# Performance work log

Measured on AMD Instinct MI355X. Metric: run time of the kernel, lower is better.

## Reference

```python
import jax, jax.numpy as jnp
import numpy as np

B, S, E, H = 2, 2048, 1024, 16
D = E // H


def setup_inputs() -> dict:
    key = jax.random.key(0)
    ks = jax.random.split(key, 12)
    init = lambda k, shp: (jax.random.normal(k, shp, dtype=jnp.float32) * 0.02)
    return {
        "q": jax.random.normal(ks[0], (B, S, E), dtype=jnp.float32),
        "k": jax.random.normal(ks[1], (B, S, E), dtype=jnp.float32),
        "v": jax.random.normal(ks[2], (B, S, E), dtype=jnp.float32),
        "wq": init(ks[3], (E, E)), "bq": jnp.zeros((E,), jnp.float32),
        "wk": init(ks[4], (E, E)), "bk": jnp.zeros((E,), jnp.float32),
        "wv": init(ks[5], (E, E)), "bv": jnp.zeros((E,), jnp.float32),
        "wo": init(ks[6], (E, E)), "bo": jnp.zeros((E,), jnp.float32),
        "gamma": jnp.ones((E,), jnp.float32),
        "beta": jnp.zeros((E,), jnp.float32),
        "mask": 1,
    }


def _split_heads(x):
    # [B,S,E] -> [B,H,S,D]
    return x.reshape(x.shape[0], x.shape[1], H, D).transpose(0, 2, 1, 3)


def _mha(q, k, v, wq, bq, wk, bk, wv, bv, wo, bo, gamma, beta, causal):
    residual = q
    query = _split_heads(q @ wq + bq)
    key = _split_heads(k @ wk + bk)
    value = _split_heads(v @ wv + bv)
    scale = jnp.sqrt(jnp.float32(D)) + 1e-8  # matches torch: sqrt(dk) + 1e-8
    score = jnp.einsum("bhqd,bhkd->bhqk", query, key) / scale
    if causal:
        cm = jnp.tril(jnp.ones((S, S), dtype=bool))  # 1 - triu(...,1)
        score = jnp.where(cm[None, None], score, -jnp.inf)
    attn = jax.nn.softmax(score, axis=-1)
    ctx = jnp.einsum("bhqk,bhkd->bhqd", attn, value)
    ctx = ctx.transpose(0, 2, 1, 3).reshape(ctx.shape[0], S, E)
    o = ctx @ wo + bo  # dropout is identity in eval mode
    x = residual + o
    mu = jnp.mean(x, axis=-1, keepdims=True)
    var = jnp.var(x, axis=-1, keepdims=True)
    return (x - mu) / jnp.sqrt(var + 1e-5) * gamma + beta


def reference(q, k, v, wq, bq, wk, bk, wv, bv, wo, bo, gamma, beta, mask):
    return _mha(q, k, v, wq, bq, wk, bk, wv, bv, wo, bo, gamma, beta, bool(mask))
```

## Files before the change

kernel.cpp:

```cpp
#include <hip/hip_runtime.h>
#include <hip/hip_bf16.h>

typedef __bf16 bf16x8 __attribute__((ext_vector_type(8)));
typedef __attribute__((ext_vector_type(8))) short short8_t;
typedef __attribute__((ext_vector_type(4))) short short4_t;
typedef __attribute__((ext_vector_type(4))) float f32x4;

#define DEV __device__ __forceinline__

constexpr int Bc = 2, Sc = 2048, Ec = 1024, Hc = 16, Dc = 64;
constexpr int Mc = Bc * Sc;
constexpr int NT = Sc / 64;
constexpr float kQS = (float)((1.0 / (8.0 + 1e-8)) * 1.4426950408889634);

DEV short f2bf(float f) {
  unsigned int u = __builtin_bit_cast(unsigned int, f);
  unsigned int r = u + 0x7fffu + ((u >> 16) & 1u);
  return (short)(r >> 16);
}
DEV short bfc(float f) { __bf16 h = (__bf16)f; return __builtin_bit_cast(short, h); }

DEV float fexp2(float x) {
#if __has_builtin(__builtin_amdgcn_exp2f)
  return __builtin_amdgcn_exp2f(x);
#else
  float r;
  asm("v_exp_f32 %0, %1" : "=v"(r) : "v"(x));
  return r;
#endif
}

DEV void gload16(const short* g, short* lds) {
  __builtin_amdgcn_global_load_lds((const __attribute__((address_space(1))) void*)g,
                                   (__attribute__((address_space(3))) void*)lds, 16, 0, 0);
}

struct Prep {
  const float* w[4]; short* wt[4];
  const float* x[3]; short* y[3];
};
__global__ __launch_bounds__(256) void k_prep(Prep a) {
  const int bid = blockIdx.x;
  if (bid < 4096) {
    __shared__ float tile[32][33];
    const int z = bid >> 10, bk = (bid >> 5) & 31, bn = bid & 31;
    const float* w = a.w[z];
    short* wt = a.wt[z];
    int tx = threadIdx.x & 31, ty = threadIdx.x >> 5;
#pragma unroll
    for (int i = 0; i < 4; i++)
      tile[ty + i * 8][tx] = w[(size_t)(bk * 32 + ty + i * 8) * Ec + bn * 32 + tx];
    __syncthreads();
#pragma unroll
    for (int i = 0; i < 4; i++)
      wt[(size_t)(bn * 32 + ty + i * 8) * Ec + bk * 32 + tx] = f2bf(tile[tx][ty + i * 8]);
  } else {
    const int idx = bid - 4096;
    const int z = idx >> 11, c = idx & 2047;
    const float* x = a.x[z];
    short* y = a.y[z];
    size_t i = ((size_t)c * 256 + threadIdx.x) * 8;
    float4 v0 = *(const float4*)(x + i);
    float4 v1 = *(const float4*)(x + i + 4);
    short8_t h;
    h[0] = bfc(v0.x); h[1] = bfc(v0.y); h[2] = bfc(v0.z); h[3] = bfc(v0.w);
    h[4] = bfc(v1.x); h[5] = bfc(v1.y); h[6] = bfc(v1.z); h[7] = bfc(v1.w);
    *(short8_t*)(y + i) = h;
  }
}

DEV void gemm_mfma(const short* lA, const short* lB, f32x4 (&acc)[4][4], int lane, int wm, int wn) {
#pragma unroll
  for (int kc = 0; kc < 2; kc++) {
    bf16x8 a[4], b[4];
#pragma unroll
    for (int mf = 0; mf < 4; mf++) {
      int row = wm * 64 + mf * 16 + (lane & 15);
      int ch = (kc * 4 + (lane >> 4)) ^ (row & 7);
      a[mf] = *(const bf16x8*)&lA[row * 64 + (ch << 3)];
    }
#pragma unroll
    for (int nf = 0; nf < 4; nf++) {
      int row = wn * 64 + nf * 16 + (lane & 15);
      int ch = (kc * 4 + (lane >> 4)) ^ (row & 7);
      b[nf] = *(const bf16x8*)&lB[row * 64 + (ch << 3)];
    }
#pragma unroll
    for (int mf = 0; mf < 4; mf++)
#pragma unroll
      for (int nf = 0; nf < 4; nf++)
        acc[mf][nf] = __builtin_amdgcn_mfma_f32_16x16x32_bf16(a[mf], b[nf], acc[mf][nf], 0, 0, 0);
  }
}

struct QKV3 { const short* A[3]; const short* Bt[3]; const float* bias[3]; short* out[3]; };

__global__ __launch_bounds__(256) void k_gemm_qkv(QKV3 args) {
  __shared__ short lA[2][128 * 64];
  __shared__ short lB[2][128 * 64];
  int lin = blockIdx.x + 8 * blockIdx.y + 256 * blockIdx.z;
  lin = (lin & 7) * 96 + (lin >> 3);
  const int bx = lin & 7, by = (lin >> 3) & 31, z = lin >> 8;
  const short* A = args.A[z];
  const short* Bt = args.Bt[z];
  const float* bias = args.bias[z];
  short* out = args.out[z];
  const int t = threadIdx.x;
  const int m0 = by * 128, n0 = bx * 128;
  const int lane = t & 63, wid = t >> 6;
  const int wm = wid >> 1, wn = wid & 1;
  const int rl = lane >> 3, chs = ((lane & 7) ^ rl) << 3;

  f32x4 acc[4][4];
#pragma unroll
  for (int i = 0; i < 4; i++)
#pragma unroll
    for (int j = 0; j < 4; j++) acc[i][j] = {0.f, 0.f, 0.f, 0.f};

  auto stage = [&](int k0, int buf) {
#pragma unroll
    for (int j = 0; j < 4; j++) {
      int r0 = wid * 32 + j * 8;
      gload16(A + (size_t)(m0 + r0 + rl) * Ec + k0 + chs, &lA[buf][r0 * 64]);
      gload16(Bt + (size_t)(n0 + r0 + rl) * Ec + k0 + chs, &lB[buf][r0 * 64]);
    }
  };
  stage(0, 0);
  __syncthreads();
  int buf = 0;
  for (int s = 0; s < Ec / 64; s++) {
    if (s + 1 < Ec / 64) stage((s + 1) * 64, buf ^ 1);
    gemm_mfma(lA[buf], lB[buf], acc, lane, wm, wn);
    __syncthreads();
    buf ^= 1;
  }
#pragma unroll
  for (int mf = 0; mf < 4; mf++) {
#pragma unroll
    for (int nf = 0; nf < 4; nf++) {
      int col = n0 + wn * 64 + nf * 16 + (lane & 15);
      float bs = bias[col];
      int row0 = m0 + wm * 64 + mf * 16 + ((lane >> 4) << 2);
      int bh = ((row0 >> 11) << 4) + (col >> 6);
      int d = col & 63;
      size_t bhbase = (size_t)bh * Sc * Dc;
      if (z == 0) {
#pragma unroll
        for (int r = 0; r < 4; r++) {
          int row = row0 + r;
          size_t off = bhbase + (size_t)(row & 2047) * Dc + d;
          out[off] = f2bf((acc[mf][nf][r] + bs) * kQS);
        }
      } else if (z == 1) {
#pragma unroll
        for (int r = 0; r < 4; r++) {
          int s = (row0 + r) & 2047;
          size_t off = bhbase + (size_t)(s >> 4) * 1024 + ((d >> 5) * 512) +
                       (((d >> 3) & 3) * 128) + ((s & 15) * 8) + (d & 7);
          out[off] = f2bf(acc[mf][nf][r] + bs);
        }
      } else {
        short4_t h;
#pragma unroll
        for (int r = 0; r < 4; r++) h[r] = f2bf(acc[mf][nf][r] + bs);
        int s0 = row0 & 2047;
        size_t off = bhbase + (size_t)(s0 >> 6) * 4096 + (((s0 >> 5) & 1) * 2048) +
                     (((d >> 4) & 3) * 512) + ((((s0 >> 3) & 3) * 16 + (d & 15)) * 8) + (s0 & 7);
        *(short4_t*)&out[off] = h;
      }
    }
  }
}

__global__ __launch_bounds__(256) void k_gemm_o(const short* __restrict__ A,
                                                const short* __restrict__ Bt,
                                                const float* __restrict__ bias,
                                                const float* __restrict__ res,
                                                float* __restrict__ out) {
  __shared__ short lA[2][128 * 64];
  __shared__ short lB[2][128 * 64];
  int lin = blockIdx.x + 8 * blockIdx.y;
  lin = (lin & 7) * 32 + (lin >> 3);
  const int bx = lin & 7, by = lin >> 3;
  const int t = threadIdx.x;
  const int m0 = by * 128, n0 = bx * 128;
  const int lane = t & 63, wid = t >> 6;
  const int wm = wid >> 1, wn = wid & 1;
  const int rl = lane >> 3, chs = ((lane & 7) ^ rl) << 3;

  f32x4 acc[4][4];
#pragma unroll
  for (int i = 0; i < 4; i++)
#pragma unroll
    for (int j = 0; j < 4; j++) acc[i][j] = {0.f, 0.f, 0.f, 0.f};

  auto stage = [&](int k0, int buf) {
#pragma unroll
    for (int j = 0; j < 4; j++) {
      int r0 = wid * 32 + j * 8;
      gload16(A + (size_t)(m0 + r0 + rl) * Ec + k0 + chs, &lA[buf][r0 * 64]);
      gload16(Bt + (size_t)(n0 + r0 + rl) * Ec + k0 + chs, &lB[buf][r0 * 64]);
    }
  };
  stage(0, 0);
  __syncthreads();
  int buf = 0;
  for (int s = 0; s < Ec / 64; s++) {
    if (s + 1 < Ec / 64) stage((s + 1) * 64, buf ^ 1);
    gemm_mfma(lA[buf], lB[buf], acc, lane, wm, wn);
    __syncthreads();
    buf ^= 1;
  }
#pragma unroll
  for (int mf = 0; mf < 4; mf++) {
#pragma unroll
    for (int nf = 0; nf < 4; nf++) {
      int col = n0 + wn * 64 + nf * 16 + (lane & 15);
      float bs = bias[col];
#pragma unroll
      for (int r = 0; r < 4; r++) {
        int row = m0 + wm * 64 + mf * 16 + ((lane >> 4) << 2) + r;
        out[(size_t)row * Ec + col] = acc[mf][nf][r] + bs + res[(size_t)row * Ec + col];
      }
    }
  }
}

__global__ __launch_bounds__(256, 3) void k_attn7(const short* __restrict__ Qp,
                                                  const short* __restrict__ Kf,
                                                  const short* __restrict__ Vf,
                                                  const int* __restrict__ maskp,
                                                  short* __restrict__ ctx) {
  __shared__ short lP[64 * 64];
  const int lin = blockIdx.x;
  const int bh = lin & 31;
  const int qtord = lin >> 5;
  const int qt = (qtord & 8) ? (qtord ^ 7) : qtord;
  const int t = threadIdx.x, lane = t & 63, w = t >> 6;
  const int gs = lane >> 4, l15 = lane & 15;
  const bool causal = maskp[0] != 0;
  const int b = bh >> 4, h = bh & 15;
  const size_t base = (size_t)bh * Sc * Dc;
  const int ktend = causal ? qt : (NT - 1);

  bf16x8 aq[2];
  {
    const short* qptr = Qp + base + (size_t)(qt * 64 + w * 16 + l15) * Dc + gs * 8;
    aq[0] = *(const bf16x8*)(qptr);
    aq[1] = *(const bf16x8*)(qptr + 32);
  }
  bf16x8 ones;
#pragma unroll
  for (int j = 0; j < 8; j++) ones[j] = (__bf16)1.0f;

  f32x4 oacc[4], lsum;
#pragma unroll
  for (int i = 0; i < 4; i++) oacc[i] = {0.f, 0.f, 0.f, 0.f};
  lsum = {0.f, 0.f, 0.f, 0.f};

  const int prow = w * 16 + l15, pswz = l15 & 7;
  short* pw[4];
  const short* pr[2];
#pragma unroll
  for (int mf = 0; mf < 4; mf++)
    pw[mf] = &lP[prow * 64 + (((2 * mf + (gs >> 1)) ^ pswz) << 3) + (gs & 1) * 4];
#pragma unroll
  for (int kc = 0; kc < 2; kc++)
    pr[kc] = &lP[prow * 64 + (((kc * 4 + gs) ^ pswz) << 3)];

  const short* Kb = Kf + base + lane * 8;
  const short* Vb = Vf + base + lane * 8;
  const int qloc = w * 16 + l15;

  bf16x8 kA[2][4], kB[2][4];
  {
#pragma unroll
    for (int mf = 0; mf < 4; mf++) {
      kA[0][mf] = *(const bf16x8*)(Kb + mf * 1024);
      kA[1][mf] = *(const bf16x8*)(Kb + mf * 1024 + 512);
    }
  }

  int kt = 0;
  auto body = [&](bf16x8 (&kc_)[2][4], bf16x8 (&kn_)[2][4]) {
    if (kt < ktend) {
      const short* kp = Kb + (kt + 1) * 4096;
#pragma unroll
      for (int mf = 0; mf < 4; mf++) {
        kn_[0][mf] = *(const bf16x8*)(kp + mf * 1024);
        kn_[1][mf] = *(const bf16x8*)(kp + mf * 1024 + 512);
      }
    }
    const short* vp = Vb + kt * 4096;
    bf16x8 vf[2][4];
#pragma unroll
    for (int c2 = 0; c2 < 2; c2++)
#pragma unroll
      for (int df = 0; df < 4; df++)
        vf[c2][df] = *(const bf16x8*)(vp + c2 * 2048 + df * 512);
    __builtin_amdgcn_sched_barrier(0);

    f32x4 s[4];
#pragma unroll
    for (int mf = 0; mf < 4; mf++) s[mf] = {0.f, 0.f, 0.f, 0.f};
#pragma unroll
    for (int c2 = 0; c2 < 2; c2++)
#pragma unroll
      for (int mf = 0; mf < 4; mf++)
        s[mf] = __builtin_amdgcn_mfma_f32_16x16x32_bf16(kc_[c2][mf], aq[c2], s[mf], 0, 0, 0);

    if (causal && kt == qt) {
#pragma unroll
      for (int mf = 0; mf < 4; mf++) {
        short4_t hh;
#pragma unroll
        for (int r = 0; r < 4; r++) {
          float p = fexp2(s[mf][r]);
          if ((mf * 16 + gs * 4 + r) > qloc) p = 0.f;
          hh[r] = bfc(p);
        }
        *(short4_t*)pw[mf] = hh;
      }
    } else {
#pragma unroll
      for (int mf = 0; mf < 4; mf++) {
        short4_t hh;
#pragma unroll
        for (int r = 0; r < 4; r++) hh[r] = bfc(fexp2(s[mf][r]));
        *(short4_t*)pw[mf] = hh;
      }
    }

    bf16x8 pa[2];
    pa[0] = *(const bf16x8*)pr[0];
    pa[1] = *(const bf16x8*)pr[1];
#pragma unroll
    for (int c2 = 0; c2 < 2; c2++) {
      lsum = __builtin_amdgcn_mfma_f32_16x16x32_bf16(pa[c2], ones, lsum, 0, 0, 0);
#pragma unroll
      for (int df = 0; df < 4; df++)
        oacc[df] = __builtin_amdgcn_mfma_f32_16x16x32_bf16(pa[c2], vf[c2][df], oacc[df], 0, 0, 0);
    }
  };

  while (true) {
    body(kA, kB);
    if (++kt > ktend) break;
    body(kB, kA);
    if (++kt > ktend) break;
  }

#pragma unroll
  for (int r = 0; r < 4; r++) {
    float ib = 1.0f / lsum[r];
    int sr = qt * 64 + w * 16 + (gs << 2) + r;
#pragma unroll
    for (int df = 0; df < 4; df++) {
      int col = h * 64 + df * 16 + l15;
      ctx[(size_t)(b * Sc + sr) * Ec + col] = f2bf(oacc[df][r] * ib);
    }
  }
}

__global__ __launch_bounds__(256) void k_ln(float* __restrict__ x,
                                            const float* __restrict__ gamma,
                                            const float* __restrict__ beta) {
  int row = blockIdx.x, t = threadIdx.x;
  float4 v = *(const float4*)(x + (size_t)row * Ec + t * 4);
  float s = v.x + v.y + v.z + v.w;
  float sq = v.x * v.x + v.y * v.y + v.z * v.z + v.w * v.w;
#pragma unroll
  for (int m = 1; m < 64; m <<= 1) {
    s += __shfl_xor(s, m);
    sq += __shfl_xor(sq, m);
  }
  __shared__ float red[8];
  if ((t & 63) == 0) {
    red[t >> 6] = s;
    red[4 + (t >> 6)] = sq;
  }
  __syncthreads();
  s = red[0] + red[1] + red[2] + red[3];
  sq = red[4] + red[5] + red[6] + red[7];
  float mu = s * (1.f / Ec);
  float var = sq * (1.f / Ec) - mu * mu;
  float rstd = rsqrtf(var + 1e-5f);
  float4 g = *(const float4*)(gamma + t * 4);
  float4 bb = *(const float4*)(beta + t * 4);
  v.x = (v.x - mu) * rstd * g.x + bb.x;
  v.y = (v.y - mu) * rstd * g.y + bb.y;
  v.z = (v.z - mu) * rstd * g.z + bb.z;
  v.w = (v.w - mu) * rstd * g.w + bb.w;
  *(float4*)(x + (size_t)row * Ec + t * 4) = v;
}

extern "C" void kernel_launch(void* const* d_in, const int* in_sizes, int n_in,
                              void* d_out, int out_size, void* d_ws, size_t ws_size,
                              hipStream_t stream) {
  const float* q = (const float*)d_in[0];
  const float* k = (const float*)d_in[1];
  const float* v = (const float*)d_in[2];
  const float* wq = (const float*)d_in[3];
  const float* bq = (const float*)d_in[4];
  const float* wk = (const float*)d_in[5];
  const float* bk = (const float*)d_in[6];
  const float* wv = (const float*)d_in[7];
  const float* bv = (const float*)d_in[8];
  const float* wo = (const float*)d_in[9];
  const float* bo = (const float*)d_in[10];
  const float* gamma = (const float*)d_in[11];
  const float* beta = (const float*)d_in[12];
  const int* maskp = (const int*)d_in[13];
  float* out = (float*)d_out;

  short* wtq = (short*)d_ws;
  short* wtk = wtq + (size_t)Ec * Ec;
  short* wtv = wtk + (size_t)Ec * Ec;
  short* wto = wtv + (size_t)Ec * Ec;
  short* Qp = wto + (size_t)Ec * Ec;
  short* Kf = Qp + (size_t)Mc * Ec;
  short* Vf = Kf + (size_t)Mc * Ec;
  short* ctx = Vf + (size_t)Mc * Ec;

  short* xq = (short*)d_out;
  short* xk = xq + (size_t)Mc * Ec;
  short* xv = ctx;

  dim3 tb(256);

  Prep pargs;
  pargs.w[0] = wq; pargs.w[1] = wk; pargs.w[2] = wv; pargs.w[3] = wo;
  pargs.wt[0] = wtq; pargs.wt[1] = wtk; pargs.wt[2] = wtv; pargs.wt[3] = wto;
  pargs.x[0] = q; pargs.x[1] = k; pargs.x[2] = v;
  pargs.y[0] = xq; pargs.y[1] = xk; pargs.y[2] = xv;
  k_prep<<<dim3(4096 + 3 * (Mc * Ec / 2048)), tb, 0, stream>>>(pargs);

  QKV3 gargs;
  gargs.A[0] = xq; gargs.A[1] = xk; gargs.A[2] = xv;
  gargs.Bt[0] = wtq; gargs.Bt[1] = wtk; gargs.Bt[2] = wtv;
  gargs.bias[0] = bq; gargs.bias[1] = bk; gargs.bias[2] = bv;
  gargs.out[0] = Qp; gargs.out[1] = Kf; gargs.out[2] = Vf;
  k_gemm_qkv<<<dim3(Ec / 128, Mc / 128, 3), tb, 0, stream>>>(gargs);

  k_attn7<<<dim3(NT * Bc * Hc), tb, 0, stream>>>(Qp, Kf, Vf, maskp, ctx);

  k_gemm_o<<<dim3(Ec / 128, Mc / 128), tb, 0, stream>>>(ctx, wto, bo, q, out);

  k_ln<<<dim3(Mc), tb, 0, stream>>>(out, gamma, beta);
}
```

Baseline: 133.0 us.

## Fuse fp32-to-bf16 input conversion into QKV GEMM A-tile loading

The separate conversion of q, k and v to bf16 in the prep kernel is removed. The QKV GEMM now reads fp32 activations directly, converts them in registers and writes swizzled bf16 tiles into LDS, which saves a full write and re-read of the converted inputs. Both GEMMs also drop LDS double buffering for single buffering with occupancy hints, relying on more resident blocks to hide latency. Load latency is no longer overlapped with compute inside a block, and the fp32 A reads double the bytes each QKV block fetches.

```diff
diff --git a/kernel.cpp b/kernel.cpp
--- a/kernel.cpp
+++ b/kernel.cpp
@@ -35,38 +35,21 @@
                                    (__attribute__((address_space(3))) void*)lds, 16, 0, 0);
 }
 
-struct Prep {
-  const float* w[4]; short* wt[4];
-  const float* x[3]; short* y[3];
-};
+struct Prep { const float* w[4]; short* wt[4]; };
 __global__ __launch_bounds__(256) void k_prep(Prep a) {
+  __shared__ float tile[32][33];
   const int bid = blockIdx.x;
-  if (bid < 4096) {
-    __shared__ float tile[32][33];
-    const int z = bid >> 10, bk = (bid >> 5) & 31, bn = bid & 31;
-    const float* w = a.w[z];
-    short* wt = a.wt[z];
-    int tx = threadIdx.x & 31, ty = threadIdx.x >> 5;
-#pragma unroll
-    for (int i = 0; i < 4; i++)
-      tile[ty + i * 8][tx] = w[(size_t)(bk * 32 + ty + i * 8) * Ec + bn * 32 + tx];
-    __syncthreads();
-#pragma unroll
-    for (int i = 0; i < 4; i++)
-      wt[(size_t)(bn * 32 + ty + i * 8) * Ec + bk * 32 + tx] = f2bf(tile[tx][ty + i * 8]);
-  } else {
-    const int idx = bid - 4096;
-    const int z = idx >> 11, c = idx & 2047;
-    const float* x = a.x[z];
-    short* y = a.y[z];
-    size_t i = ((size_t)c * 256 + threadIdx.x) * 8;
-    float4 v0 = *(const float4*)(x + i);
-    float4 v1 = *(const float4*)(x + i + 4);
-    short8_t h;
-    h[0] = bfc(v0.x); h[1] = bfc(v0.y); h[2] = bfc(v0.z); h[3] = bfc(v0.w);
-    h[4] = bfc(v1.x); h[5] = bfc(v1.y); h[6] = bfc(v1.z); h[7] = bfc(v1.w);
-    *(short8_t*)(y + i) = h;
-  }
+  const int z = bid >> 10, bk = (bid >> 5) & 31, bn = bid & 31;
+  const float* w = a.w[z];
+  short* wt = a.wt[z];
+  int tx = threadIdx.x & 31, ty = threadIdx.x >> 5;
+#pragma unroll
+  for (int i = 0; i < 4; i++)
+    tile[ty + i * 8][tx] = w[(size_t)(bk * 32 + ty + i * 8) * Ec + bn * 32 + tx];
+  __syncthreads();
+#pragma unroll
+  for (int i = 0; i < 4; i++)
+    wt[(size_t)(bn * 32 + ty + i * 8) * Ec + bk * 32 + tx] = f2bf(tile[tx][ty + i * 8]);
 }
 
 DEV void gemm_mfma(const short* lA, const short* lB, f32x4 (&acc)[4][4], int lane, int wm, int wn) {
@@ -93,15 +76,15 @@
   }
 }
 
-struct QKV3 { const short* A[3]; const short* Bt[3]; const float* bias[3]; short* out[3]; };
-
-__global__ __launch_bounds__(256) void k_gemm_qkv(QKV3 args) {
-  __shared__ short lA[2][128 * 64];
-  __shared__ short lB[2][128 * 64];
+struct QKV3 { const float* A[3]; const short* Bt[3]; const float* bias[3]; short* out[3]; };
+
+__global__ __launch_bounds__(256, 3) void k_gemm_qkv(QKV3 args) {
+  __shared__ short lA[128 * 64];
+  __shared__ short lB[128 * 64];
   int lin = blockIdx.x + 8 * blockIdx.y + 256 * blockIdx.z;
   lin = (lin & 7) * 96 + (lin >> 3);
   const int bx = lin & 7, by = (lin >> 3) & 31, z = lin >> 8;
-  const short* A = args.A[z];
+  const float* A = args.A[z];
   const short* Bt = args.Bt[z];
   const float* bias = args.bias[z];
   short* out = args.out[z];
@@ -110,6 +93,10 @@
   const int lane = t & 63, wid = t >> 6;
   const int wm = wid >> 1, wn = wid & 1;
   const int rl = lane >> 3, chs = ((lane & 7) ^ rl) << 3;
+  const int arow = t >> 1, acs = (t & 1) * 4;
+  const float* arp0 = A + (size_t)(m0 + arow) * Ec + (t & 1) * 32;
+  short* awp = &lA[arow * 64];
+  const int aswz = arow & 7;
 
   f32x4 acc[4][4];
 #pragma unroll
@@ -117,22 +104,29 @@
 #pragma unroll
     for (int j = 0; j < 4; j++) acc[i][j] = {0.f, 0.f, 0.f, 0.f};
 
-  auto stage = [&](int k0, int buf) {
+  for (int s = 0; s < Ec / 64; s++) {
+    const int k0 = s * 64;
+    const float* arp = arp0 + k0;
+    float4 av[8];
+#pragma unroll
+    for (int j = 0; j < 8; j++) av[j] = *(const float4*)(arp + j * 4);
 #pragma unroll
     for (int j = 0; j < 4; j++) {
       int r0 = wid * 32 + j * 8;
-      gload16(A + (size_t)(m0 + r0 + rl) * Ec + k0 + chs, &lA[buf][r0 * 64]);
-      gload16(Bt + (size_t)(n0 + r0 + rl) * Ec + k0 + chs, &lB[buf][r0 * 64]);
-    }
-  };
-  stage(0, 0);
-  __syncthreads();
-  int buf = 0;
-  for (int s = 0; s < Ec / 64; s++) {
-    if (s + 1 < Ec / 64) stage((s + 1) * 64, buf ^ 1);
-    gemm_mfma(lA[buf], lB[buf], acc, lane, wm, wn);
+      gload16(Bt + (size_t)(n0 + r0 + rl) * Ec + k0 + chs, &lB[r0 * 64]);
+    }
+#pragma unroll
+    for (int j = 0; j < 4; j++) {
+      short8_t h;
+      h[0] = bfc(av[2 * j].x); h[1] = bfc(av[2 * j].y);
+      h[2] = bfc(av[2 * j].z); h[3] = bfc(av[2 * j].w);
+      h[4] = bfc(av[2 * j + 1].x); h[5] = bfc(av[2 * j + 1].y);
+      h[6] = bfc(av[2 * j + 1].z); h[7] = bfc(av[2 * j + 1].w);
+      *(short8_t*)&awp[(((acs + j) ^ aswz) << 3)] = h;
+    }
     __syncthreads();
-    buf ^= 1;
+    gemm_mfma(lA, lB, acc, lane, wm, wn);
+    __syncthreads();
   }
 #pragma unroll
   for (int mf = 0; mf < 4; mf++) {
@@ -154,9 +148,9 @@
       } else if (z == 1) {
 #pragma unroll
         for (int r = 0; r < 4; r++) {
-          int s = (row0 + r) & 2047;
-          size_t off = bhbase + (size_t)(s >> 4) * 1024 + ((d >> 5) * 512) +
-                       (((d >> 3) & 3) * 128) + ((s & 15) * 8) + (d & 7);
+          int sr = (row0 + r) & 2047;
+          size_t off = bhbase + (size_t)(sr >> 4) * 1024 + ((d >> 5) * 512) +
+                       (((d >> 3) & 3) * 128) + ((sr & 15) * 8) + (d & 7);
           out[off] = f2bf(acc[mf][nf][r] + bs);
         }
       } else {
@@ -172,13 +166,13 @@
   }
 }
 
-__global__ __launch_bounds__(256) void k_gemm_o(const short* __restrict__ A,
-                                                const short* __restrict__ Bt,
-                                                const float* __restrict__ bias,
-                                                const float* __restrict__ res,
-                                                float* __restrict__ out) {
-  __shared__ short lA[2][128 * 64];
-  __shared__ short lB[2][128 * 64];
+__global__ __launch_bounds__(256, 4) void k_gemm_o(const short* __restrict__ A,
+                                                   const short* __restrict__ Bt,
+                                                   const float* __restrict__ bias,
+                                                   const float* __restrict__ res,
+                                                   float* __restrict__ out) {
+  __shared__ short lA[128 * 64];
+  __shared__ short lB[128 * 64];
   int lin = blockIdx.x + 8 * blockIdx.y;
   lin = (lin & 7) * 32 + (lin >> 3);
   const int bx = lin & 7, by = lin >> 3;
@@ -194,22 +188,17 @@
 #pragma unroll
     for (int j = 0; j < 4; j++) acc[i][j] = {0.f, 0.f, 0.f, 0.f};
 
-  auto stage = [&](int k0, int buf) {
+  for (int s = 0; s < Ec / 64; s++) {
+    const int k0 = s * 64;
 #pragma unroll
     for (int j = 0; j < 4; j++) {
       int r0 = wid * 32 + j * 8;
-      gload16(A + (size_t)(m0 + r0 + rl) * Ec + k0 + chs, &lA[buf][r0 * 64]);
-      gload16(Bt + (size_t)(n0 + r0 + rl) * Ec + k0 + chs, &lB[buf][r0 * 64]);
-    }
-  };
-  stage(0, 0);
-  __syncthreads();
-  int buf = 0;
-  for (int s = 0; s < Ec / 64; s++) {
-    if (s + 1 < Ec / 64) stage((s + 1) * 64, buf ^ 1);
-    gemm_mfma(lA[buf], lB[buf], acc, lane, wm, wn);
+      gload16(A + (size_t)(m0 + r0 + rl) * Ec + k0 + chs, &lA[r0 * 64]);
+      gload16(Bt + (size_t)(n0 + r0 + rl) * Ec + k0 + chs, &lB[r0 * 64]);
+    }
     __syncthreads();
-    buf ^= 1;
+    gemm_mfma(lA, lB, acc, lane, wm, wn);
+    __syncthreads();
   }
 #pragma unroll
   for (int mf = 0; mf < 4; mf++) {
@@ -422,21 +411,15 @@
   short* Vf = Kf + (size_t)Mc * Ec;
   short* ctx = Vf + (size_t)Mc * Ec;
 
-  short* xq = (short*)d_out;
-  short* xk = xq + (size_t)Mc * Ec;
-  short* xv = ctx;
-
   dim3 tb(256);
 
   Prep pargs;
   pargs.w[0] = wq; pargs.w[1] = wk; pargs.w[2] = wv; pargs.w[3] = wo;
   pargs.wt[0] = wtq; pargs.wt[1] = wtk; pargs.wt[2] = wtv; pargs.wt[3] = wto;
-  pargs.x[0] = q; pargs.x[1] = k; pargs.x[2] = v;
-  pargs.y[0] = xq; pargs.y[1] = xk; pargs.y[2] = xv;
-  k_prep<<<dim3(4096 + 3 * (Mc * Ec / 2048)), tb, 0, stream>>>(pargs);
+  k_prep<<<dim3(4096), tb, 0, stream>>>(pargs);
 
   QKV3 gargs;
-  gargs.A[0] = xq; gargs.A[1] = xk; gargs.A[2] = xv;
+  gargs.A[0] = q; gargs.A[1] = k; gargs.A[2] = v;
   gargs.Bt[0] = wtq; gargs.Bt[1] = wtk; gargs.Bt[2] = wtv;
   gargs.bias[0] = bq; gargs.bias[1] = bk; gargs.bias[2] = bv;
   gargs.out[0] = Qp; gargs.out[1] = Kf; gargs.out[2] = Vf;
```

After: 145.4 us. 9.3% more time.
